# Optimization experiments

Measured on AMD Instinct MI355X. Metric: run time of the kernel, lower is better.

The kernel has to match this reference:

```python
import jax, jax.numpy as jnp
import numpy as np

LEN = 8388608  # 2**23, must be a power of 2


def setup_inputs() -> dict:
    key = jax.random.key(0)
    k1, k2 = jax.random.split(key)
    inp = jax.random.normal(k1, (LEN,), dtype=jnp.float32)
    weight = jax.random.uniform(k2, (LEN // 2, 2), dtype=jnp.float32)  # learned twiddle factors
    return {"input": inp, "weight": weight}


def _complex_mul(a, w):
    # a: [d, cols, 2] complex pairs; w: [cols, 2] broadcast over leading dim
    ar, ai = a[:, :, 0], a[:, :, 1]
    wr, wi = w[:, 0], w[:, 1]
    return jnp.stack([ar * wr - ai * wi, ar * wi + ai * wr], axis=-1)


def reference(input, weight):
    n = input.shape[0]
    # real signal -> complex pairs, shape [n, 1, 2]
    x = jnp.stack([input, jnp.zeros_like(input)], axis=-1)[:, None, :]
    d = n // 2
    while d != 0:  # log2(n) static stages
        w = weight[0::d]          # [cols, 2] where cols == x.shape[1]
        top = x[:d]               # [d, cols, 2]
        bot = x[d:]               # [d, cols, 2]
        p = _complex_mul(bot, w)  # butterfly twiddle multiply
        x = jnp.concatenate([top + p, top - p], axis=1)  # [d, 2*cols, 2]
        d //= 2
    return x  # [1, n, 2]
```

## Files before the change

### kernel.cpp

```cpp
#include <hip/hip_runtime.h>

__device__ __forceinline__ float2 cadd(float2 a, float2 b) { return make_float2(a.x + b.x, a.y + b.y); }
__device__ __forceinline__ float2 csub(float2 a, float2 b) { return make_float2(a.x - b.x, a.y - b.y); }
__device__ __forceinline__ float2 cmul(float2 w, float2 z) {
    return make_float2(w.x * z.x - w.y * z.y, w.x * z.y + w.y * z.x);
}


__global__ __launch_bounds__(256) void fft_pass_a(const float* __restrict__ in,
                                                  const float2* __restrict__ wt,
                                                  float2* __restrict__ out)
{
    __shared__ float2 L[256 * 16];
    const int tid = threadIdx.x;
    const int l0  = blockIdx.x << 4;

    {
        const int c4 = tid & 3;
        const int gg = tid >> 2;
#pragma unroll
        for (int k = 0; k < 4; ++k) {
            const int g = gg + (k << 6);
            const float4 v = *reinterpret_cast<const float4*>(in + ((size_t)g << 15) + l0 + (c4 << 2));
            const int base = (g << 4) + (c4 << 2);
            L[base + 0] = make_float2(v.x, 0.f);
            L[base + 1] = make_float2(v.y, 0.f);
            L[base + 2] = make_float2(v.z, 0.f);
            L[base + 3] = make_float2(v.w, 0.f);
        }
    }
    __syncthreads();

    const int c  = tid & 15;
    const int qb = tid >> 4;
#pragma unroll
    for (int rho = 0; rho < 4; ++rho) {
        const int s  = rho << 1;
        const int H  = 128 >> s;
        const int Q  = H >> 1;
        const int lo = 6 - s;
#pragma unroll
        for (int k = 0; k < 4; ++k) {
            const int qi = (qb << 2) + k;
            const int b  = ((qi >> lo) << (lo + 2)) | (qi & ((1 << lo) - 1));
            const int jloc = s ? (int)(__brev((unsigned)(b >> (8 - s))) >> (32 - s)) : 0;
            const int e  = jloc << (21 - s);
            const float2 w2a = wt[e];
            const float2 w1  = wt[e << 1];
            const float2 w2b = wt[e + (1 << 21)];
            const int iA = (b << 4) + c;
            const float2 A  = L[iA];
            const float2 Bv = L[iA + (Q << 4)];
            const float2 Cv = L[iA + (H << 4)];
            const float2 Dv = L[iA + ((H + Q) << 4)];
            const float2 pC = cmul(w1, Cv), pD = cmul(w1, Dv);
            const float2 tA = cadd(A, pC),  tC = csub(A, pC);
            const float2 tB = cadd(Bv, pD), tD = csub(Bv, pD);
            const float2 p2 = cmul(w2a, tB);
            const float2 p3 = cmul(w2b, tD);
            L[iA]                  = cadd(tA, p2);
            L[iA + (Q << 4)]       = csub(tA, p2);
            L[iA + (H << 4)]       = cadd(tC, p3);
            L[iA + ((H + Q) << 4)] = csub(tC, p3);
        }
        __syncthreads();
    }

    {
        const int c2 = tid & 7;
        const int gg = tid >> 3;
#pragma unroll
        for (int k = 0; k < 8; ++k) {
            const int g  = gg + (k << 5);
            const int li = (g << 4) + (c2 << 1);
            const float2 a0 = L[li], a1 = L[li + 1];
            *reinterpret_cast<float4*>(out + ((size_t)g << 15) + l0 + (c2 << 1)) =
                make_float4(a0.x, a0.y, a1.x, a1.y);
        }
    }
}

__global__ __launch_bounds__(256) void fft_pass_b(const float2* __restrict__ in,
                                                  const float2* __restrict__ wt,
                                                  float2* __restrict__ out)
{
    __shared__ float2 L[256 * 16];
    const int tid  = threadIdx.x;
    const int h    = blockIdx.x >> 3;
    const int l0   = (blockIdx.x & 7) << 4;
    const size_t base = ((size_t)h << 15) + l0;
    const int hrev = (int)(__brev((unsigned)h) >> 24);

    {
        const int c2 = tid & 7;
        const int gg = tid >> 3;
#pragma unroll
        for (int k = 0; k < 8; ++k) {
            const int g = gg + (k << 5);
            const float4 v = *reinterpret_cast<const float4*>(in + base + (g << 7) + (c2 << 1));
            const int li = (g << 4) + (c2 << 1);
            L[li]     = make_float2(v.x, v.y);
            L[li + 1] = make_float2(v.z, v.w);
        }
    }
    __syncthreads();

    const int c  = tid & 15;
    const int qb = tid >> 4;
#pragma unroll
    for (int rho = 0; rho < 4; ++rho) {
        const int s  = rho << 1;
        const int H  = 128 >> s;
        const int Q  = H >> 1;
        const int lo = 6 - s;
#pragma unroll
        for (int k = 0; k < 4; ++k) {
            const int qi = (qb << 2) + k;
            const int b  = ((qi >> lo) << (lo + 2)) | (qi & ((1 << lo) - 1));
            const int jloc = s ? (int)(__brev((unsigned)(b >> (8 - s))) >> (32 - s)) : 0;
            const int e  = (hrev << (13 - s)) + (jloc << (21 - s));
            const float2 w2a = wt[e];
            const float2 w1  = wt[e << 1];
            const float2 w2b = wt[e + (1 << 21)];
            const int iA = (b << 4) + c;
            const float2 A  = L[iA];
            const float2 Bv = L[iA + (Q << 4)];
            const float2 Cv = L[iA + (H << 4)];
            const float2 Dv = L[iA + ((H + Q) << 4)];
            const float2 pC = cmul(w1, Cv), pD = cmul(w1, Dv);
            const float2 tA = cadd(A, pC),  tC = csub(A, pC);
            const float2 tB = cadd(Bv, pD), tD = csub(Bv, pD);
            const float2 p2 = cmul(w2a, tB);
            const float2 p3 = cmul(w2b, tD);
            L[iA]                  = cadd(tA, p2);
            L[iA + (Q << 4)]       = csub(tA, p2);
            L[iA + (H << 4)]       = cadd(tC, p3);
            L[iA + ((H + Q) << 4)] = csub(tC, p3);
        }
        __syncthreads();
    }

    {
        const int c2 = tid & 7;
        const int gg = tid >> 3;
#pragma unroll
        for (int k = 0; k < 8; ++k) {
            const int g  = gg + (k << 5);
            const int li = (g << 4) + (c2 << 1);
            const float2 a0 = L[li], a1 = L[li + 1];
            *reinterpret_cast<float4*>(out + base + (g << 7) + (c2 << 1)) =
                make_float4(a0.x, a0.y, a1.x, a1.y);
        }
    }
}

__global__ __launch_bounds__(256) void fft_pass_c(const float2* __restrict__ in,
                                                  const float2* __restrict__ wt,
                                                  float2* __restrict__ out)
{
    __shared__ float2 L[64 * 129];
    const int tid = threadIdx.x;
    const int h0  = blockIdx.x;

    {
        const int f  = tid & 63;
        const int ll = tid >> 6;
#pragma unroll
        for (int k = 0; k < 16; ++k) {
            const int lam = ll + (k << 2);
            const int H   = (int)(__brev((unsigned)((h0 << 6) + lam)) >> 16);
            const float4 v = *reinterpret_cast<const float4*>(in + ((size_t)H << 7) + (f << 1));
            const int li = lam * 129 + (f << 1);
            L[li]     = make_float2(v.x, v.y);
            L[li + 1] = make_float2(v.z, v.w);
        }
    }
    __syncthreads();

    const int lam = tid & 63;
    const int qh  = tid >> 6;
    const int rH  = (h0 << 6) + lam;
#pragma unroll
    for (int rho = 0; rho < 3; ++rho) {
        const int s  = rho << 1;
        const int H  = 64 >> s;
        const int Q  = H >> 1;
        const int lo = 5 - s;
#pragma unroll
        for (int k = 0; k < 8; ++k) {
            const int qi = (qh << 3) + k;
            const int b  = ((qi >> lo) << (lo + 2)) | (qi & ((1 << lo) - 1));
            const int jloc = s ? (int)(__brev((unsigned)(b >> (7 - s))) >> (32 - s)) : 0;
            const int e  = (rH << (5 - s)) + (jloc << (21 - s));
            const float2 w2a = wt[e];
            const float2 w1  = wt[e << 1];
            const float2 w2b = wt[e + (1 << 21)];
            const int iA = lam * 129 + b;
            const float2 A  = L[iA];
            const float2 Bv = L[iA + Q];
            const float2 Cv = L[iA + H];
            const float2 Dv = L[iA + H + Q];
            const float2 pC = cmul(w1, Cv), pD = cmul(w1, Dv);
            const float2 tA = cadd(A, pC),  tC = csub(A, pC);
            const float2 tB = cadd(Bv, pD), tD = csub(Bv, pD);
            const float2 p2 = cmul(w2a, tB);
            const float2 p3 = cmul(w2b, tD);
            L[iA]         = cadd(tA, p2);
            L[iA + Q]     = csub(tA, p2);
            L[iA + H]     = cadd(tC, p3);
            L[iA + H + Q] = csub(tC, p3);
        }
        __syncthreads();
    }

    {
#pragma unroll
        for (int k = 0; k < 16; ++k) {
            const int pb   = (qh << 4) + k;
            const int b    = pb << 1;
            const int jloc = (int)(__brev((unsigned)pb) >> 26);
            const float2 w = wt[rH + (jloc << 16)];
            const int iA = lam * 129 + b;
            const float2 A  = L[iA];
            const float2 Bv = L[iA + 1];
            const float2 p  = cmul(w, Bv);
            L[iA]     = cadd(A, p);
            L[iA + 1] = csub(A, p);
        }
    }
    __syncthreads();

    {
        const int l2 = (tid & 31) << 1;
        const int gb = tid >> 5;
#pragma unroll
        for (int k = 0; k < 16; ++k) {
            const int g    = gb + (k << 3);
            const int grev = (int)(__brev((unsigned)g) >> 25);
            const float2 a0 = L[l2 * 129 + g];
            const float2 a1 = L[(l2 + 1) * 129 + g];
            const size_t o = ((size_t)grev << 16) + (h0 << 6) + l2;
            *reinterpret_cast<float4*>(out + o) = make_float4(a0.x, a0.y, a1.x, a1.y);
        }
    }
}

extern "C" void kernel_launch(void* const* d_in, const int* in_sizes, int n_in,
                              void* d_out, int out_size, void* d_ws, size_t ws_size,
                              hipStream_t stream)
{
    (void)in_sizes; (void)n_in; (void)out_size; (void)ws_size;
    const float*  in = (const float*)d_in[0];
    const float2* wt = (const float2*)d_in[1];
    float2* outc = (float2*)d_out;
    float2* wsc  = (float2*)d_ws;

    fft_pass_a<<<2048, 256, 0, stream>>>(in, wt, outc);
    fft_pass_b<<<2048, 256, 0, stream>>>(outc, wt, wsc);
    fft_pass_c<<<1024, 256, 0, stream>>>(wsc, wt, outc);
}
```

Before: 207.6 us.

## Prefetch next-stage twiddles into registers and halve pass C block size

Each radix-4 stage now loads the next stage's twiddle factors into registers before doing the current stage's butterflies, so global twiddle loads overlap LDS work and barriers. The first stage's twiddles are loaded before the initial tile load. Pass C is re-tiled to 32 rows per block with twice as many blocks, halving LDS use and raising occupancy, and its final radix-2 twiddles are prefetched too. Keeping the prefetched twiddles in registers raises register pressure.

```diff
diff --git a/kernel.cpp b/kernel.cpp
--- a/kernel.cpp
+++ b/kernel.cpp
@@ -11,13 +11,18 @@
                                                   const float2* __restrict__ wt,
                                                   float2* __restrict__ out)
 {
-    __shared__ float2 L[256 * 16];
+    __shared__ float2 L[4096];
     const int tid = threadIdx.x;
     const int l0  = blockIdx.x << 4;
-
-    {
-        const int c4 = tid & 3;
-        const int gg = tid >> 2;
+    const int c   = tid & 15;
+    const int qb  = tid >> 4;
+
+    float2 pw1[4], pw2a[4], pw2b[4];
+#pragma unroll
+    for (int k = 0; k < 4; ++k) { pw1[k] = wt[0]; pw2a[k] = wt[0]; pw2b[k] = wt[1 << 21]; }
+
+    {
+        const int c4 = tid & 3, gg = tid >> 2;
 #pragma unroll
         for (int k = 0; k < 4; ++k) {
             const int g = gg + (k << 6);
@@ -31,44 +36,49 @@
     }
     __syncthreads();
 
-    const int c  = tid & 15;
-    const int qb = tid >> 4;
 #pragma unroll
     for (int rho = 0; rho < 4; ++rho) {
-        const int s  = rho << 1;
-        const int H  = 128 >> s;
-        const int Q  = H >> 1;
-        const int lo = 6 - s;
+        const int s = rho << 1, H = 128 >> s, Q = H >> 1, lo = 6 - s;
+        float2 nw1[4], nw2a[4], nw2b[4];
+        if (rho < 3) {
+            const int s2 = s + 2, lo2 = 6 - s2;
+#pragma unroll
+            for (int k = 0; k < 4; ++k) {
+                const int qi = (qb << 2) + k;
+                const int b  = ((qi >> lo2) << (lo2 + 2)) | (qi & ((1 << lo2) - 1));
+                const int jl = (int)(__brev((unsigned)(b >> (8 - s2))) >> (32 - s2));
+                const int e  = jl << (21 - s2);
+                nw1[k] = wt[e << 1]; nw2a[k] = wt[e]; nw2b[k] = wt[e + (1 << 21)];
+            }
+        }
 #pragma unroll
         for (int k = 0; k < 4; ++k) {
             const int qi = (qb << 2) + k;
             const int b  = ((qi >> lo) << (lo + 2)) | (qi & ((1 << lo) - 1));
-            const int jloc = s ? (int)(__brev((unsigned)(b >> (8 - s))) >> (32 - s)) : 0;
-            const int e  = jloc << (21 - s);
-            const float2 w2a = wt[e];
-            const float2 w1  = wt[e << 1];
-            const float2 w2b = wt[e + (1 << 21)];
             const int iA = (b << 4) + c;
             const float2 A  = L[iA];
             const float2 Bv = L[iA + (Q << 4)];
             const float2 Cv = L[iA + (H << 4)];
             const float2 Dv = L[iA + ((H + Q) << 4)];
-            const float2 pC = cmul(w1, Cv), pD = cmul(w1, Dv);
+            const float2 pC = cmul(pw1[k], Cv), pD = cmul(pw1[k], Dv);
             const float2 tA = cadd(A, pC),  tC = csub(A, pC);
             const float2 tB = cadd(Bv, pD), tD = csub(Bv, pD);
-            const float2 p2 = cmul(w2a, tB);
-            const float2 p3 = cmul(w2b, tD);
+            const float2 p2 = cmul(pw2a[k], tB);
+            const float2 p3 = cmul(pw2b[k], tD);
             L[iA]                  = cadd(tA, p2);
             L[iA + (Q << 4)]       = csub(tA, p2);
             L[iA + (H << 4)]       = cadd(tC, p3);
             L[iA + ((H + Q) << 4)] = csub(tC, p3);
         }
         __syncthreads();
-    }
-
-    {
-        const int c2 = tid & 7;
-        const int gg = tid >> 3;
+        if (rho < 3) {
+#pragma unroll
+            for (int k = 0; k < 4; ++k) { pw1[k] = nw1[k]; pw2a[k] = nw2a[k]; pw2b[k] = nw2b[k]; }
+        }
+    }
+
+    {
+        const int c2 = tid & 7, gg = tid >> 3;
 #pragma unroll
         for (int k = 0; k < 8; ++k) {
             const int g  = gg + (k << 5);
@@ -84,16 +94,24 @@
                                                   const float2* __restrict__ wt,
                                                   float2* __restrict__ out)
 {
-    __shared__ float2 L[256 * 16];
+    __shared__ float2 L[4096];
     const int tid  = threadIdx.x;
     const int h    = blockIdx.x >> 3;
     const int l0   = (blockIdx.x & 7) << 4;
     const size_t base = ((size_t)h << 15) + l0;
     const int hrev = (int)(__brev((unsigned)h) >> 24);
-
-    {
-        const int c2 = tid & 7;
-        const int gg = tid >> 3;
+    const int c  = tid & 15;
+    const int qb = tid >> 4;
+
+    float2 pw1[4], pw2a[4], pw2b[4];
+    {
+        const int e0 = hrev << 13;
+#pragma unroll
+        for (int k = 0; k < 4; ++k) { pw1[k] = wt[e0 << 1]; pw2a[k] = wt[e0]; pw2b[k] = wt[e0 + (1 << 21)]; }
+    }
+
+    {
+        const int c2 = tid & 7, gg = tid >> 3;
 #pragma unroll
         for (int k = 0; k < 8; ++k) {
             const int g = gg + (k << 5);
@@ -105,44 +123,49 @@
     }
     __syncthreads();
 
-    const int c  = tid & 15;
-    const int qb = tid >> 4;
 #pragma unroll
     for (int rho = 0; rho < 4; ++rho) {
-        const int s  = rho << 1;
-        const int H  = 128 >> s;
-        const int Q  = H >> 1;
-        const int lo = 6 - s;
+        const int s = rho << 1, H = 128 >> s, Q = H >> 1, lo = 6 - s;
+        float2 nw1[4], nw2a[4], nw2b[4];
+        if (rho < 3) {
+            const int s2 = s + 2, lo2 = 6 - s2;
+#pragma unroll
+            for (int k = 0; k < 4; ++k) {
+                const int qi = (qb << 2) + k;
+                const int b  = ((qi >> lo2) << (lo2 + 2)) | (qi & ((1 << lo2) - 1));
+                const int jl = (int)(__brev((unsigned)(b >> (8 - s2))) >> (32 - s2));
+                const int e  = (hrev << (13 - s2)) + (jl << (21 - s2));
+                nw1[k] = wt[e << 1]; nw2a[k] = wt[e]; nw2b[k] = wt[e + (1 << 21)];
+            }
+        }
 #pragma unroll
         for (int k = 0; k < 4; ++k) {
             const int qi = (qb << 2) + k;
             const int b  = ((qi >> lo) << (lo + 2)) | (qi & ((1 << lo) - 1));
-            const int jloc = s ? (int)(__brev((unsigned)(b >> (8 - s))) >> (32 - s)) : 0;
-            const int e  = (hrev << (13 - s)) + (jloc << (21 - s));
-            const float2 w2a = wt[e];
-            const float2 w1  = wt[e << 1];
-            const float2 w2b = wt[e + (1 << 21)];
             const int iA = (b << 4) + c;
             const float2 A  = L[iA];
             const float2 Bv = L[iA + (Q << 4)];
             const float2 Cv = L[iA + (H << 4)];
             const float2 Dv = L[iA + ((H + Q) << 4)];
-            const float2 pC = cmul(w1, Cv), pD = cmul(w1, Dv);
+            const float2 pC = cmul(pw1[k], Cv), pD = cmul(pw1[k], Dv);
             const float2 tA = cadd(A, pC),  tC = csub(A, pC);
             const float2 tB = cadd(Bv, pD), tD = csub(Bv, pD);
-            const float2 p2 = cmul(w2a, tB);
-            const float2 p3 = cmul(w2b, tD);
+            const float2 p2 = cmul(pw2a[k], tB);
+            const float2 p3 = cmul(pw2b[k], tD);
             L[iA]                  = cadd(tA, p2);
             L[iA + (Q << 4)]       = csub(tA, p2);
             L[iA + (H << 4)]       = cadd(tC, p3);
             L[iA + ((H + Q) << 4)] = csub(tC, p3);
         }
         __syncthreads();
-    }
-
-    {
-        const int c2 = tid & 7;
-        const int gg = tid >> 3;
+        if (rho < 3) {
+#pragma unroll
+            for (int k = 0; k < 4; ++k) { pw1[k] = nw1[k]; pw2a[k] = nw2a[k]; pw2b[k] = nw2b[k]; }
+        }
+    }
+
+    {
+        const int c2 = tid & 7, gg = tid >> 3;
 #pragma unroll
         for (int k = 0; k < 8; ++k) {
             const int g  = gg + (k << 5);
@@ -158,72 +181,95 @@
                                                   const float2* __restrict__ wt,
                                                   float2* __restrict__ out)
 {
-    __shared__ float2 L[64 * 129];
+    __shared__ float2 L[32 * 129];
     const int tid = threadIdx.x;
     const int h0  = blockIdx.x;
 
+    const int lam = tid & 31;
+    const int bq  = tid >> 5;
+    const int rH  = (h0 << 5) + lam;
+
+    float2 pw1[4], pw2a[4], pw2b[4];
+#pragma unroll
+    for (int k = 0; k < 4; ++k) {
+        pw1[k]  = wt[rH << 6];
+        pw2a[k] = wt[rH << 5];
+        pw2b[k] = wt[(rH << 5) + (1 << 21)];
+    }
+
     {
         const int f  = tid & 63;
         const int ll = tid >> 6;
 #pragma unroll
-        for (int k = 0; k < 16; ++k) {
-            const int lam = ll + (k << 2);
-            const int H   = (int)(__brev((unsigned)((h0 << 6) + lam)) >> 16);
+        for (int k = 0; k < 8; ++k) {
+            const int lm = ll + (k << 2);
+            const int H  = (int)(__brev((unsigned)((h0 << 5) + lm)) >> 16);
             const float4 v = *reinterpret_cast<const float4*>(in + ((size_t)H << 7) + (f << 1));
-            const int li = lam * 129 + (f << 1);
+            const int li = lm * 129 + (f << 1);
             L[li]     = make_float2(v.x, v.y);
             L[li + 1] = make_float2(v.z, v.w);
         }
     }
     __syncthreads();
 
-    const int lam = tid & 63;
-    const int qh  = tid >> 6;
-    const int rH  = (h0 << 6) + lam;
+    float2 pr2[8];
 #pragma unroll
     for (int rho = 0; rho < 3; ++rho) {
-        const int s  = rho << 1;
-        const int H  = 64 >> s;
-        const int Q  = H >> 1;
-        const int lo = 5 - s;
-#pragma unroll
-        for (int k = 0; k < 8; ++k) {
-            const int qi = (qh << 3) + k;
+        const int s = rho << 1, H = 64 >> s, Q = H >> 1, lo = 5 - s;
+        float2 nw1[4], nw2a[4], nw2b[4];
+        if (rho < 2) {
+            const int s2 = s + 2, lo2 = 5 - s2;
+#pragma unroll
+            for (int k = 0; k < 4; ++k) {
+                const int qi = (bq << 2) + k;
+                const int b  = ((qi >> lo2) << (lo2 + 2)) | (qi & ((1 << lo2) - 1));
+                const int jl = (int)(__brev((unsigned)(b >> (7 - s2))) >> (32 - s2));
+                const int e  = (rH << (5 - s2)) + (jl << (21 - s2));
+                nw1[k] = wt[e << 1]; nw2a[k] = wt[e]; nw2b[k] = wt[e + (1 << 21)];
+            }
+        } else {
+#pragma unroll
+            for (int k = 0; k < 8; ++k) {
+                const int pb = (bq << 3) + k;
+                const int jl = (int)(__brev((unsigned)pb) >> 26);
+                pr2[k] = wt[rH + (jl << 16)];
+            }
+        }
+#pragma unroll
+        for (int k = 0; k < 4; ++k) {
+            const int qi = (bq << 2) + k;
             const int b  = ((qi >> lo) << (lo + 2)) | (qi & ((1 << lo) - 1));
-            const int jloc = s ? (int)(__brev((unsigned)(b >> (7 - s))) >> (32 - s)) : 0;
-            const int e  = (rH << (5 - s)) + (jloc << (21 - s));
-            const float2 w2a = wt[e];
-            const float2 w1  = wt[e << 1];
-            const float2 w2b = wt[e + (1 << 21)];
             const int iA = lam * 129 + b;
             const float2 A  = L[iA];
             const float2 Bv = L[iA + Q];
             const float2 Cv = L[iA + H];
             const float2 Dv = L[iA + H + Q];
-            const float2 pC = cmul(w1, Cv), pD = cmul(w1, Dv);
+            const float2 pC = cmul(pw1[k], Cv), pD = cmul(pw1[k], Dv);
             const float2 tA = cadd(A, pC),  tC = csub(A, pC);
             const float2 tB = cadd(Bv, pD), tD = csub(Bv, pD);
-            const float2 p2 = cmul(w2a, tB);
-            const float2 p3 = cmul(w2b, tD);
+            const float2 p2 = cmul(pw2a[k], tB);
+            const float2 p3 = cmul(pw2b[k], tD);
             L[iA]         = cadd(tA, p2);
             L[iA + Q]     = csub(tA, p2);
             L[iA + H]     = cadd(tC, p3);
             L[iA + H + Q] = csub(tC, p3);
         }
         __syncthreads();
-    }
-
-    {
-#pragma unroll
-        for (int k = 0; k < 16; ++k) {
-            const int pb   = (qh << 4) + k;
-            const int b    = pb << 1;
-            const int jloc = (int)(__brev((unsigned)pb) >> 26);
-            const float2 w = wt[rH + (jloc << 16)];
+        if (rho < 2) {
+#pragma unroll
+            for (int k = 0; k < 4; ++k) { pw1[k] = nw1[k]; pw2a[k] = nw2a[k]; pw2b[k] = nw2b[k]; }
+        }
+    }
+
+    {
+#pragma unroll
+        for (int k = 0; k < 8; ++k) {
+            const int pb = (bq << 3) + k;
+            const int b  = pb << 1;
             const int iA = lam * 129 + b;
             const float2 A  = L[iA];
             const float2 Bv = L[iA + 1];
-            const float2 p  = cmul(w, Bv);
+            const float2 p  = cmul(pr2[k], Bv);
             L[iA]     = cadd(A, p);
             L[iA + 1] = csub(A, p);
         }
@@ -231,15 +277,15 @@
     __syncthreads();
 
     {
-        const int l2 = (tid & 31) << 1;
-        const int gb = tid >> 5;
-#pragma unroll
-        for (int k = 0; k < 16; ++k) {
-            const int g    = gb + (k << 3);
+        const int l2 = (tid & 15) << 1;
+        const int gb = tid >> 4;
+#pragma unroll
+        for (int k = 0; k < 8; ++k) {
+            const int g    = gb + (k << 4);
             const int grev = (int)(__brev((unsigned)g) >> 25);
             const float2 a0 = L[l2 * 129 + g];
             const float2 a1 = L[(l2 + 1) * 129 + g];
-            const size_t o = ((size_t)grev << 16) + (h0 << 6) + l2;
+            const size_t o = ((size_t)grev << 16) + (h0 << 5) + l2;
             *reinterpret_cast<float4*>(out + o) = make_float4(a0.x, a0.y, a1.x, a1.y);
         }
     }
@@ -257,5 +303,5 @@
 
     fft_pass_a<<<2048, 256, 0, stream>>>(in, wt, outc);
     fft_pass_b<<<2048, 256, 0, stream>>>(outc, wt, wsc);
-    fft_pass_c<<<1024, 256, 0, stream>>>(wsc, wt, outc);
-}
+    fft_pass_c<<<2048, 256, 0, stream>>>(wsc, wt, outc);
+}
```

New measurement: 198.6 us. 4.4% less time.
